# Kernel tuning notes

Measured on AMD Instinct MI355X. Metric: run time of the kernel, lower is better.

## Reference

```python
import jax, jax.numpy as jnp
import numpy as np

N_NODES = 100000
N_EDGES = 1600000
D_IN = 128
D_HID = 128
GARMENT_SIZE = 80000


def setup_inputs() -> dict:
    key = jax.random.key(0)
    k1, k2, k3, k4, k5, k6 = jax.random.split(key, 6)
    notes = jax.random.normal(k1, (N_NODES, D_IN), dtype=jnp.float32)
    w = jax.random.normal(k2, (D_IN, D_HID), dtype=jnp.float32) * 0.05
    b = jax.random.normal(k3, (D_HID,), dtype=jnp.float32) * 0.05
    edge_src = jax.random.randint(k4, (N_EDGES,), 0, N_NODES, dtype=jnp.int32)
    edge_dst = jax.random.randint(k5, (N_EDGES,), 0, N_NODES, dtype=jnp.int32)
    edge_w = jax.random.uniform(k6, (N_EDGES,), dtype=jnp.float32)
    return {
        "notes": notes,
        "w": w,
        "b": b,
        "edge_src": edge_src,
        "edge_dst": edge_dst,
        "edge_w": edge_w,
        "garment_size": GARMENT_SIZE,
    }


def reference(notes, w, b, edge_src, edge_dst, edge_w, garment_size):
    # Dense projection: X0 = notes @ w   -> [N, H]
    X0 = jnp.einsum("nd,dh->nh", notes, w)
    # edge_convolution_template(edge_function=lambda x, y: y, reduction='weighted'):
    # X1[i] = sum over edges (i -> j) of a_ij * X0[j]
    msgs = X0[edge_dst] * edge_w[:, None]                      # [E, H] gather + scale
    X1 = jax.ops.segment_sum(msgs, edge_src, num_segments=notes.shape[0])  # [N, H]
    X = X1 + b
    # concat(act(X), X0[garment_size:]) along node axis -> [2N - garment_size, H]
    return jnp.concatenate([jax.nn.relu(X), X0[garment_size:]], axis=0)
```

## Files before the change

### kernel.cpp

```cpp
#include <hip/hip_runtime.h>

#define H 128
#define NPB 256
#define NB_MAX 1024
#define FILL_CH 4096

static __device__ __forceinline__ unsigned short f2bf(float f) {
  unsigned u = __float_as_uint(f);
  u += 0x7FFFu + ((u >> 16) & 1u);
  return (unsigned short)(u >> 16);
}

__global__ __launch_bounds__(256) void gemm_kernel(
    const float* __restrict__ notes, const float* __restrict__ w,
    const int* __restrict__ g_ptr, unsigned short* __restrict__ x0h,
    float* __restrict__ out, int n_nodes) {
  __shared__ float wtile[32 * H];
  __shared__ float ntile[64 * 32];
  const int tid = threadIdx.x;
  const int tx = tid & 31;
  const int ty = tid >> 5;
  const int rowBlk = blockIdx.x * 64;
  const int g = *g_ptr;

  float acc[8][4];
#pragma unroll
  for (int i = 0; i < 8; ++i)
#pragma unroll
    for (int j = 0; j < 4; ++j) acc[i][j] = 0.f;

  for (int kc = 0; kc < H; kc += 32) {
    __syncthreads();
    {
      const float4* wg = (const float4*)(w + (size_t)kc * H);
      float4* wl = (float4*)wtile;
#pragma unroll
      for (int i = 0; i < 4; ++i) wl[tid + i * 256] = wg[tid + i * 256];
    }
    {
      float4* nl = (float4*)ntile;
#pragma unroll
      for (int i = 0; i < 2; ++i) {
        const int idx = tid + i * 256;
        const int row = idx >> 3;
        const int q = idx & 7;
        const int rr = min(rowBlk + row, n_nodes - 1);
        nl[idx] = *(const float4*)(notes + (size_t)rr * H + kc + q * 4);
      }
    }
    __syncthreads();
#pragma unroll 8
    for (int kk = 0; kk < 32; ++kk) {
      const float4 b4 = *(const float4*)&wtile[kk * H + tx * 4];
      float a[8];
#pragma unroll
      for (int i = 0; i < 8; ++i) a[i] = ntile[(ty * 8 + i) * 32 + kk];
#pragma unroll
      for (int i = 0; i < 8; ++i) {
        acc[i][0] += a[i] * b4.x;
        acc[i][1] += a[i] * b4.y;
        acc[i][2] += a[i] * b4.z;
        acc[i][3] += a[i] * b4.w;
      }
    }
  }

#pragma unroll
  for (int i = 0; i < 8; ++i) {
    const int r = rowBlk + ty * 8 + i;
    if (r < n_nodes) {
      ushort4 h;
      h.x = f2bf(acc[i][0]);
      h.y = f2bf(acc[i][1]);
      h.z = f2bf(acc[i][2]);
      h.w = f2bf(acc[i][3]);
      *(ushort4*)(x0h + (size_t)r * H + tx * 4) = h;
      if (r >= g) {
        float4 v;
        v.x = acc[i][0]; v.y = acc[i][1]; v.z = acc[i][2]; v.w = acc[i][3];
        *(float4*)(out + (size_t)(n_nodes + r - g) * H + tx * 4) = v;
      }
    }
  }
}

__global__ __launch_bounds__(256) void bucket_count_kernel(
    const int* __restrict__ esrc, int* __restrict__ bucketCount, int n_edges,
    int nb) {
  __shared__ int cnt[NB_MAX];
  for (int i = threadIdx.x; i < nb; i += 256) cnt[i] = 0;
  __syncthreads();
  int i = blockIdx.x * 256 + threadIdx.x;
  const int stride = gridDim.x * 256;
  for (; i < n_edges; i += stride) atomicAdd(&cnt[esrc[i] >> 8], 1);
  __syncthreads();
  for (int j = threadIdx.x; j < nb; j += 256) {
    const int c = cnt[j];
    if (c) atomicAdd(&bucketCount[j], c);
  }
}

__global__ __launch_bounds__(256) void bucket_scan_kernel(
    const int* __restrict__ bucketCount, int* __restrict__ bucketBase,
    int* __restrict__ bucketCursor, int* __restrict__ off, int nb,
    int n_nodes, int n_edges) {
  __shared__ int part[256];
  const int t = threadIdx.x;
  const int K = (nb + 255) / 256;
  const int lo = t * K;
  const int hi = min(lo + K, nb);
  int sum = 0;
  for (int i = lo; i < hi; ++i) sum += bucketCount[i];
  part[t] = sum;
  __syncthreads();
  for (int o = 1; o < 256; o <<= 1) {
    const int tv = (t >= o) ? part[t - o] : 0;
    __syncthreads();
    part[t] += tv;
    __syncthreads();
  }
  int run = (t == 0) ? 0 : part[t - 1];
  for (int i = lo; i < hi; ++i) {
    bucketBase[i] = run;
    bucketCursor[i] = run;
    run += bucketCount[i];
  }
  if (t == 255) {
    bucketBase[nb] = part[255];
    off[n_nodes] = n_edges;
  }
}

__global__ __launch_bounds__(256) void bucket_fill_kernel(
    const int* __restrict__ esrc, const int* __restrict__ edst,
    const float* __restrict__ ew, int* __restrict__ bucketCursor,
    int2* __restrict__ sedge, unsigned char* __restrict__ srcloc, int n_edges,
    int nb) {
  __shared__ int2 stage[FILL_CH];
  __shared__ unsigned short bkt16[FILL_CH];
  __shared__ unsigned char loc8[FILL_CH];
  __shared__ int cntA[NB_MAX];
  __shared__ int lbase[NB_MAX];
  __shared__ int cntC[NB_MAX];
  const int t = threadIdx.x;
  const int base = blockIdx.x * FILL_CH;
  const int edgesInBlock = min(FILL_CH, n_edges - base);

  for (int i = t; i < nb; i += 256) {
    cntA[i] = 0;
    cntC[i] = 0;
  }
  __syncthreads();

  for (int k = 0; k < FILL_CH / 256; ++k) {
    const int e = base + k * 256 + t;
    if (e < n_edges) atomicAdd(&cntA[esrc[e] >> 8], 1);
  }
  __syncthreads();

  {
    __shared__ int part[256];
    const int K = (nb + 255) / 256;
    const int lo = t * K;
    const int hi = min(lo + K, nb);
    int sum = 0;
    for (int i = lo; i < hi; ++i) sum += cntA[i];
    part[t] = sum;
    __syncthreads();
    for (int o = 1; o < 256; o <<= 1) {
      const int tv = (t >= o) ? part[t - o] : 0;
      __syncthreads();
      part[t] += tv;
      __syncthreads();
    }
    int run = (t == 0) ? 0 : part[t - 1];
    for (int i = lo; i < hi; ++i) {
      lbase[i] = run;
      run += cntA[i];
    }
  }
  __syncthreads();
  for (int i = t; i < nb; i += 256) {
    const int c = cntA[i];
    cntA[i] = c ? atomicAdd(&bucketCursor[i], c) : 0;
  }
  __syncthreads();

  for (int k = 0; k < FILL_CH / 256; ++k) {
    const int e = base + k * 256 + t;
    if (e < n_edges) {
      const int s = esrc[e];
      const int b = s >> 8;
      const int r = atomicAdd(&cntC[b], 1);
      const int sp = lbase[b] + r;
      int2 pk;
      pk.x = edst[e];
      pk.y = __float_as_int(ew[e]);
      stage[sp] = pk;
      bkt16[sp] = (unsigned short)b;
      loc8[sp] = (unsigned char)(s & 255);
    }
  }
  __syncthreads();

  for (int j = t; j < edgesInBlock; j += 256) {
    const int b = bkt16[j];
    const int pos = cntA[b] + (j - lbase[b]);
    sedge[pos] = stage[j];
    srcloc[pos] = loc8[j];
  }
}

__global__ __launch_bounds__(256) void bucket_sort_kernel(
    const int* __restrict__ bucketBase, const int2* __restrict__ sedge,
    const unsigned char* __restrict__ srcloc, int2* __restrict__ sedge2,
    int* __restrict__ off, int n_nodes) {
  __shared__ int cnt[NPB];
  __shared__ int nodeOff[NPB];
  const int t = threadIdx.x;
  const int beg = bucketBase[blockIdx.x];
  const int end = bucketBase[blockIdx.x + 1];
  const int nodeBase = blockIdx.x * NPB;
  const int nodesInBucket = min(NPB, n_nodes - nodeBase);

  cnt[t] = 0;
  __syncthreads();
  for (int j = beg + t; j < end; j += 256) atomicAdd(&cnt[srcloc[j]], 1);
  __syncthreads();
  {
    const int v = cnt[t];
    int s = v;
    nodeOff[t] = s;
    __syncthreads();
    for (int o = 1; o < 256; o <<= 1) {
      const int tv = (t >= o) ? nodeOff[t - o] : 0;
      __syncthreads();
      nodeOff[t] += tv;
      __syncthreads();
    }
    nodeOff[t] -= v;
  }
  if (t < nodesInBucket) off[nodeBase + t] = beg + nodeOff[t];
  cnt[t] = 0;
  __syncthreads();
  for (int j = beg + t; j < end; j += 256) {
    const int loc = srcloc[j];
    const int r = atomicAdd(&cnt[loc], 1);
    sedge2[beg + nodeOff[loc] + r] = sedge[j];
  }
}

__global__ __launch_bounds__(256) void gather_kernel(
    const int* __restrict__ off, const int2* __restrict__ sedge,
    const unsigned short* __restrict__ x0h, const float* __restrict__ b,
    float* __restrict__ out, int n_nodes) {
  const int wave = blockIdx.x * (blockDim.x >> 6) + (threadIdx.x >> 6);
  const int lane = threadIdx.x & 63;
  if (wave >= n_nodes) return;
  const int beg = off[wave];
  const int end = off[wave + 1];
  const unsigned* __restrict__ x0u = (const unsigned*)x0h;

  float2 a0 = {0.f, 0.f}, a1 = {0.f, 0.f};
  float2 a2 = {0.f, 0.f}, a3 = {0.f, 0.f};
  int e = beg;
  for (; e + 3 < end; e += 4) {
    const int2 e0 = sedge[e];
    const int2 e1 = sedge[e + 1];
    const int2 e2 = sedge[e + 2];
    const int2 e3 = sedge[e + 3];
    const unsigned u0 = x0u[(size_t)e0.x * 64 + lane];
    const unsigned u1 = x0u[(size_t)e1.x * 64 + lane];
    const unsigned u2 = x0u[(size_t)e2.x * 64 + lane];
    const unsigned u3 = x0u[(size_t)e3.x * 64 + lane];
    const float w0 = __int_as_float(e0.y);
    const float w1 = __int_as_float(e1.y);
    const float w2 = __int_as_float(e2.y);
    const float w3 = __int_as_float(e3.y);
    a0.x += __uint_as_float(u0 << 16) * w0;
    a0.y += __uint_as_float(u0 & 0xFFFF0000u) * w0;
    a1.x += __uint_as_float(u1 << 16) * w1;
    a1.y += __uint_as_float(u1 & 0xFFFF0000u) * w1;
    a2.x += __uint_as_float(u2 << 16) * w2;
    a2.y += __uint_as_float(u2 & 0xFFFF0000u) * w2;
    a3.x += __uint_as_float(u3 << 16) * w3;
    a3.y += __uint_as_float(u3 & 0xFFFF0000u) * w3;
  }
  for (; e < end; ++e) {
    const int2 e0 = sedge[e];
    const unsigned u0 = x0u[(size_t)e0.x * 64 + lane];
    const float w0 = __int_as_float(e0.y);
    a0.x += __uint_as_float(u0 << 16) * w0;
    a0.y += __uint_as_float(u0 & 0xFFFF0000u) * w0;
  }
  const float2 bb = ((const float2*)b)[lane];
  float2 r;
  r.x = fmaxf(a0.x + a1.x + a2.x + a3.x + bb.x, 0.f);
  r.y = fmaxf(a0.y + a1.y + a2.y + a3.y + bb.y, 0.f);
  ((float2*)out)[(size_t)wave * 64 + lane] = r;
}

__global__ __launch_bounds__(256) void scatter_kernel(
    const int* __restrict__ esrc, const int* __restrict__ edst,
    const float* __restrict__ ew, const unsigned short* __restrict__ x0h,
    float* __restrict__ acc, int n_edges) {
  const int lane = threadIdx.x & 63;
  const int waveId = blockIdx.x * (blockDim.x >> 6) + (threadIdx.x >> 6);
  const int nWaves = gridDim.x * (blockDim.x >> 6);
  const unsigned* __restrict__ x0u = (const unsigned*)x0h;
  for (int e = waveId; e < n_edges; e += nWaves) {
    const int s = esrc[e];
    const int d = edst[e];
    const float wt = ew[e];
    const unsigned u = x0u[(size_t)d * 64 + lane];
    float* p = acc + (size_t)s * H + lane * 2;
    atomicAdd(p, __uint_as_float(u << 16) * wt);
    atomicAdd(p + 1, __uint_as_float(u & 0xFFFF0000u) * wt);
  }
}

__global__ __launch_bounds__(256) void epilogue_kernel(
    float* __restrict__ out, const float* __restrict__ b, int n4) {
  const int i = blockIdx.x * blockDim.x + threadIdx.x;
  if (i >= n4) return;
  float4* o4 = (float4*)out;
  const float4* b4 = (const float4*)b;
  float4 v = o4[i];
  const float4 bb = b4[i & 31];
  v.x = fmaxf(v.x + bb.x, 0.f);
  v.y = fmaxf(v.y + bb.y, 0.f);
  v.z = fmaxf(v.z + bb.z, 0.f);
  v.w = fmaxf(v.w + bb.w, 0.f);
  o4[i] = v;
}

extern "C" void kernel_launch(void* const* d_in, const int* in_sizes, int n_in,
                              void* d_out, int out_size, void* d_ws, size_t ws_size,
                              hipStream_t stream) {
  const float* notes = (const float*)d_in[0];
  const float* w     = (const float*)d_in[1];
  const float* b     = (const float*)d_in[2];
  const int*   esrc  = (const int*)d_in[3];
  const int*   edst  = (const int*)d_in[4];
  const float* ew    = (const float*)d_in[5];
  const int*   gptr  = (const int*)d_in[6];

  const int n_nodes = in_sizes[0] / H;
  const int n_edges = in_sizes[3];
  float* out = (float*)d_out;

  const int nb = (n_nodes + NPB - 1) / NPB;

  char* ws = (char*)d_ws;
  size_t p = 0;
  auto alloc = [&](size_t bytes) -> char* {
    char* cur = ws + p;
    p = (p + bytes + 255) & ~(size_t)255;
    return cur;
  };
  unsigned short* x0h = (unsigned short*)alloc((size_t)n_nodes * H * 2);
  int*  bucketCount  = (int*)alloc((size_t)nb * sizeof(int));
  int*  bucketBase   = (int*)alloc(((size_t)nb + 1) * sizeof(int));
  int*  bucketCursor = (int*)alloc((size_t)nb * sizeof(int));
  int*  off          = (int*)alloc(((size_t)n_nodes + 1) * sizeof(int));
  int2* sedge        = (int2*)alloc((size_t)n_edges * sizeof(int2));
  int2* sedge2       = (int2*)alloc((size_t)n_edges * sizeof(int2));
  unsigned char* srcloc = (unsigned char*)alloc((size_t)n_edges);
  const bool ok = (p <= ws_size) && (nb <= NB_MAX);

  gemm_kernel<<<(n_nodes + 63) / 64, 256, 0, stream>>>(notes, w, gptr, x0h, out,
                                                       n_nodes);

  if (ok) {
    hipMemsetAsync(bucketCount, 0, (size_t)nb * sizeof(int), stream);
    bucket_count_kernel<<<256, 256, 0, stream>>>(esrc, bucketCount, n_edges,
                                                 nb);
    bucket_scan_kernel<<<1, 256, 0, stream>>>(bucketCount, bucketBase,
                                              bucketCursor, off, nb, n_nodes,
                                              n_edges);
    bucket_fill_kernel<<<(n_edges + FILL_CH - 1) / FILL_CH, 256, 0, stream>>>(
        esrc, edst, ew, bucketCursor, sedge, srcloc, n_edges, nb);
    bucket_sort_kernel<<<nb, 256, 0, stream>>>(bucketBase, sedge, srcloc,
                                               sedge2, off, n_nodes);
    gather_kernel<<<(n_nodes + 3) / 4, 256, 0, stream>>>(off, sedge2, x0h, b,
                                                         out, n_nodes);
  } else {
    hipMemsetAsync(d_out, 0, (size_t)n_nodes * H * sizeof(float), stream);
    scatter_kernel<<<2048, 256, 0, stream>>>(esrc, edst, ew, x0h, out, n_edges);
    const int n4 = n_nodes * H / 4;
    epilogue_kernel<<<(n4 + 255) / 256, 256, 0, stream>>>(out, b, n4);
  }
}
```

Baseline: 308.8 us.

## Build CSR via per-node degree atomics and direct fill; shuffle-batched gather

Replaces the two-pass bucket sort (block-local staging plus per-bucket sort) with a per-node degree histogram using global atomics, a hierarchical scan into per-node offsets, and a direct scatter of each edge into its CSR slot via an atomic cursor. This removes one full pass over an intermediate edge array and the srcloc buffer, at the cost of many global atomics on random addresses and uncoalesced writes. The gather kernel now loads 64 edge records cooperatively per wave and broadcasts them with shuffles, issuing 8 independent row loads per step to raise memory-level parallelism. The order of edges within a node becomes nondeterministic, so float summation order may vary between runs.

```diff
diff --git a/kernel.cpp b/kernel.cpp
--- a/kernel.cpp
+++ b/kernel.cpp
@@ -2,8 +2,6 @@
 
 #define H 128
 #define NPB 256
-#define NB_MAX 1024
-#define FILL_CH 4096
 
 static __device__ __forceinline__ unsigned short f2bf(float f) {
   unsigned u = __float_as_uint(f);
@@ -84,26 +82,30 @@
   }
 }
 
-__global__ __launch_bounds__(256) void bucket_count_kernel(
-    const int* __restrict__ esrc, int* __restrict__ bucketCount, int n_edges,
-    int nb) {
-  __shared__ int cnt[NB_MAX];
-  for (int i = threadIdx.x; i < nb; i += 256) cnt[i] = 0;
+__global__ __launch_bounds__(256) void deg_count_kernel(
+    const int* __restrict__ esrc, int* __restrict__ deg, int n_edges) {
+  const int i = blockIdx.x * 256 + threadIdx.x;
+  if (i >= n_edges) return;
+  atomicAdd(&deg[esrc[i]], 1);
+}
+
+__global__ __launch_bounds__(256) void bucket_sum_kernel(
+    const int* __restrict__ deg, int* __restrict__ bucketCount, int n_nodes) {
+  __shared__ int red[256];
+  const int t = threadIdx.x;
+  const int node = blockIdx.x * 256 + t;
+  red[t] = (node < n_nodes) ? deg[node] : 0;
   __syncthreads();
-  int i = blockIdx.x * 256 + threadIdx.x;
-  const int stride = gridDim.x * 256;
-  for (; i < n_edges; i += stride) atomicAdd(&cnt[esrc[i] >> 8], 1);
-  __syncthreads();
-  for (int j = threadIdx.x; j < nb; j += 256) {
-    const int c = cnt[j];
-    if (c) atomicAdd(&bucketCount[j], c);
-  }
+  for (int o = 128; o > 0; o >>= 1) {
+    if (t < o) red[t] += red[t + o];
+    __syncthreads();
+  }
+  if (t == 0) bucketCount[blockIdx.x] = red[0];
 }
 
 __global__ __launch_bounds__(256) void bucket_scan_kernel(
     const int* __restrict__ bucketCount, int* __restrict__ bucketBase,
-    int* __restrict__ bucketCursor, int* __restrict__ off, int nb,
-    int n_nodes, int n_edges) {
+    int* __restrict__ off, int nb, int n_nodes, int n_edges) {
   __shared__ int part[256];
   const int t = threadIdx.x;
   const int K = (nb + 255) / 256;
@@ -122,7 +124,6 @@
   int run = (t == 0) ? 0 : part[t - 1];
   for (int i = lo; i < hi; ++i) {
     bucketBase[i] = run;
-    bucketCursor[i] = run;
     run += bucketCount[i];
   }
   if (t == 255) {
@@ -131,123 +132,40 @@
   }
 }
 
-__global__ __launch_bounds__(256) void bucket_fill_kernel(
+__global__ __launch_bounds__(256) void node_off_kernel(
+    const int* __restrict__ deg, const int* __restrict__ bucketBase,
+    int* __restrict__ off, int* __restrict__ cursor, int n_nodes) {
+  __shared__ int sc[256];
+  const int t = threadIdx.x;
+  const int node = blockIdx.x * 256 + t;
+  const int v = (node < n_nodes) ? deg[node] : 0;
+  sc[t] = v;
+  __syncthreads();
+  for (int o = 1; o < 256; o <<= 1) {
+    const int tv = (t >= o) ? sc[t - o] : 0;
+    __syncthreads();
+    sc[t] += tv;
+    __syncthreads();
+  }
+  if (node < n_nodes) {
+    const int o0 = bucketBase[blockIdx.x] + sc[t] - v;
+    off[node] = o0;
+    cursor[node] = o0;
+  }
+}
+
+__global__ __launch_bounds__(256) void direct_fill_kernel(
     const int* __restrict__ esrc, const int* __restrict__ edst,
-    const float* __restrict__ ew, int* __restrict__ bucketCursor,
-    int2* __restrict__ sedge, unsigned char* __restrict__ srcloc, int n_edges,
-    int nb) {
-  __shared__ int2 stage[FILL_CH];
-  __shared__ unsigned short bkt16[FILL_CH];
-  __shared__ unsigned char loc8[FILL_CH];
-  __shared__ int cntA[NB_MAX];
-  __shared__ int lbase[NB_MAX];
-  __shared__ int cntC[NB_MAX];
-  const int t = threadIdx.x;
-  const int base = blockIdx.x * FILL_CH;
-  const int edgesInBlock = min(FILL_CH, n_edges - base);
-
-  for (int i = t; i < nb; i += 256) {
-    cntA[i] = 0;
-    cntC[i] = 0;
-  }
-  __syncthreads();
-
-  for (int k = 0; k < FILL_CH / 256; ++k) {
-    const int e = base + k * 256 + t;
-    if (e < n_edges) atomicAdd(&cntA[esrc[e] >> 8], 1);
-  }
-  __syncthreads();
-
-  {
-    __shared__ int part[256];
-    const int K = (nb + 255) / 256;
-    const int lo = t * K;
-    const int hi = min(lo + K, nb);
-    int sum = 0;
-    for (int i = lo; i < hi; ++i) sum += cntA[i];
-    part[t] = sum;
-    __syncthreads();
-    for (int o = 1; o < 256; o <<= 1) {
-      const int tv = (t >= o) ? part[t - o] : 0;
-      __syncthreads();
-      part[t] += tv;
-      __syncthreads();
-    }
-    int run = (t == 0) ? 0 : part[t - 1];
-    for (int i = lo; i < hi; ++i) {
-      lbase[i] = run;
-      run += cntA[i];
-    }
-  }
-  __syncthreads();
-  for (int i = t; i < nb; i += 256) {
-    const int c = cntA[i];
-    cntA[i] = c ? atomicAdd(&bucketCursor[i], c) : 0;
-  }
-  __syncthreads();
-
-  for (int k = 0; k < FILL_CH / 256; ++k) {
-    const int e = base + k * 256 + t;
-    if (e < n_edges) {
-      const int s = esrc[e];
-      const int b = s >> 8;
-      const int r = atomicAdd(&cntC[b], 1);
-      const int sp = lbase[b] + r;
-      int2 pk;
-      pk.x = edst[e];
-      pk.y = __float_as_int(ew[e]);
-      stage[sp] = pk;
-      bkt16[sp] = (unsigned short)b;
-      loc8[sp] = (unsigned char)(s & 255);
-    }
-  }
-  __syncthreads();
-
-  for (int j = t; j < edgesInBlock; j += 256) {
-    const int b = bkt16[j];
-    const int pos = cntA[b] + (j - lbase[b]);
-    sedge[pos] = stage[j];
-    srcloc[pos] = loc8[j];
-  }
-}
-
-__global__ __launch_bounds__(256) void bucket_sort_kernel(
-    const int* __restrict__ bucketBase, const int2* __restrict__ sedge,
-    const unsigned char* __restrict__ srcloc, int2* __restrict__ sedge2,
-    int* __restrict__ off, int n_nodes) {
-  __shared__ int cnt[NPB];
-  __shared__ int nodeOff[NPB];
-  const int t = threadIdx.x;
-  const int beg = bucketBase[blockIdx.x];
-  const int end = bucketBase[blockIdx.x + 1];
-  const int nodeBase = blockIdx.x * NPB;
-  const int nodesInBucket = min(NPB, n_nodes - nodeBase);
-
-  cnt[t] = 0;
-  __syncthreads();
-  for (int j = beg + t; j < end; j += 256) atomicAdd(&cnt[srcloc[j]], 1);
-  __syncthreads();
-  {
-    const int v = cnt[t];
-    int s = v;
-    nodeOff[t] = s;
-    __syncthreads();
-    for (int o = 1; o < 256; o <<= 1) {
-      const int tv = (t >= o) ? nodeOff[t - o] : 0;
-      __syncthreads();
-      nodeOff[t] += tv;
-      __syncthreads();
-    }
-    nodeOff[t] -= v;
-  }
-  if (t < nodesInBucket) off[nodeBase + t] = beg + nodeOff[t];
-  cnt[t] = 0;
-  __syncthreads();
-  for (int j = beg + t; j < end; j += 256) {
-    const int loc = srcloc[j];
-    const int r = atomicAdd(&cnt[loc], 1);
-    sedge2[beg + nodeOff[loc] + r] = sedge[j];
-  }
+    const float* __restrict__ ew, int* __restrict__ cursor,
+    int2* __restrict__ sedge2, int n_edges) {
+  const int i = blockIdx.x * 256 + threadIdx.x;
+  if (i >= n_edges) return;
+  const int s = esrc[i];
+  const int slot = atomicAdd(&cursor[s], 1);
+  int2 pk;
+  pk.x = edst[i];
+  pk.y = __float_as_int(ew[i]);
+  sedge2[slot] = pk;
 }
 
 __global__ __launch_bounds__(256) void gather_kernel(
@@ -259,44 +177,47 @@
   if (wave >= n_nodes) return;
   const int beg = off[wave];
   const int end = off[wave + 1];
+  const int deg = end - beg;
   const unsigned* __restrict__ x0u = (const unsigned*)x0h;
 
-  float2 a0 = {0.f, 0.f}, a1 = {0.f, 0.f};
-  float2 a2 = {0.f, 0.f}, a3 = {0.f, 0.f};
-  int e = beg;
-  for (; e + 3 < end; e += 4) {
-    const int2 e0 = sedge[e];
-    const int2 e1 = sedge[e + 1];
-    const int2 e2 = sedge[e + 2];
-    const int2 e3 = sedge[e + 3];
-    const unsigned u0 = x0u[(size_t)e0.x * 64 + lane];
-    const unsigned u1 = x0u[(size_t)e1.x * 64 + lane];
-    const unsigned u2 = x0u[(size_t)e2.x * 64 + lane];
-    const unsigned u3 = x0u[(size_t)e3.x * 64 + lane];
-    const float w0 = __int_as_float(e0.y);
-    const float w1 = __int_as_float(e1.y);
-    const float w2 = __int_as_float(e2.y);
-    const float w3 = __int_as_float(e3.y);
-    a0.x += __uint_as_float(u0 << 16) * w0;
-    a0.y += __uint_as_float(u0 & 0xFFFF0000u) * w0;
-    a1.x += __uint_as_float(u1 << 16) * w1;
-    a1.y += __uint_as_float(u1 & 0xFFFF0000u) * w1;
-    a2.x += __uint_as_float(u2 << 16) * w2;
-    a2.y += __uint_as_float(u2 & 0xFFFF0000u) * w2;
-    a3.x += __uint_as_float(u3 << 16) * w3;
-    a3.y += __uint_as_float(u3 & 0xFFFF0000u) * w3;
-  }
-  for (; e < end; ++e) {
-    const int2 e0 = sedge[e];
-    const unsigned u0 = x0u[(size_t)e0.x * 64 + lane];
-    const float w0 = __int_as_float(e0.y);
-    a0.x += __uint_as_float(u0 << 16) * w0;
-    a0.y += __uint_as_float(u0 & 0xFFFF0000u) * w0;
-  }
+  float2 acc[8];
+#pragma unroll
+  for (int j = 0; j < 8; ++j) acc[j] = make_float2(0.f, 0.f);
+
+  for (int base = 0; base < deg; base += 64) {
+    const int m = min(64, deg - base);
+    const int2 md = sedge[beg + base + min(lane, m - 1)];
+    const float mw = __int_as_float(md.y);
+    for (int e = 0; e < m; e += 8) {
+      int d[8];
+      float wv[8];
+#pragma unroll
+      for (int j = 0; j < 8; ++j) {
+        const int idx = e + j;
+        const int src = min(idx, m - 1);
+        d[j] = __shfl(md.x, src);
+        const float wj = __shfl(mw, src);
+        wv[j] = (idx < m) ? wj : 0.f;
+      }
+      unsigned u[8];
+#pragma unroll
+      for (int j = 0; j < 8; ++j) u[j] = x0u[(size_t)d[j] * 64 + lane];
+#pragma unroll
+      for (int j = 0; j < 8; ++j) {
+        acc[j].x += __uint_as_float(u[j] << 16) * wv[j];
+        acc[j].y += __uint_as_float(u[j] & 0xFFFF0000u) * wv[j];
+      }
+    }
+  }
+
   const float2 bb = ((const float2*)b)[lane];
   float2 r;
-  r.x = fmaxf(a0.x + a1.x + a2.x + a3.x + bb.x, 0.f);
-  r.y = fmaxf(a0.y + a1.y + a2.y + a3.y + bb.y, 0.f);
+  r.x = fmaxf(acc[0].x + acc[1].x + acc[2].x + acc[3].x + acc[4].x + acc[5].x +
+                  acc[6].x + acc[7].x + bb.x,
+              0.f);
+  r.y = fmaxf(acc[0].y + acc[1].y + acc[2].y + acc[3].y + acc[4].y + acc[5].y +
+                  acc[6].y + acc[7].y + bb.y,
+              0.f);
   ((float2*)out)[(size_t)wave * 64 + lane] = r;
 }
 
@@ -359,29 +280,28 @@
     return cur;
   };
   unsigned short* x0h = (unsigned short*)alloc((size_t)n_nodes * H * 2);
+  int*  deg          = (int*)alloc((size_t)n_nodes * sizeof(int));
+  int*  cursor       = (int*)alloc((size_t)n_nodes * sizeof(int));
+  int*  off          = (int*)alloc(((size_t)n_nodes + 1) * sizeof(int));
   int*  bucketCount  = (int*)alloc((size_t)nb * sizeof(int));
   int*  bucketBase   = (int*)alloc(((size_t)nb + 1) * sizeof(int));
-  int*  bucketCursor = (int*)alloc((size_t)nb * sizeof(int));
-  int*  off          = (int*)alloc(((size_t)n_nodes + 1) * sizeof(int));
-  int2* sedge        = (int2*)alloc((size_t)n_edges * sizeof(int2));
   int2* sedge2       = (int2*)alloc((size_t)n_edges * sizeof(int2));
-  unsigned char* srcloc = (unsigned char*)alloc((size_t)n_edges);
-  const bool ok = (p <= ws_size) && (nb <= NB_MAX);
+  const bool ok = (p <= ws_size);
 
   gemm_kernel<<<(n_nodes + 63) / 64, 256, 0, stream>>>(notes, w, gptr, x0h, out,
                                                        n_nodes);
 
   if (ok) {
-    hipMemsetAsync(bucketCount, 0, (size_t)nb * sizeof(int), stream);
-    bucket_count_kernel<<<256, 256, 0, stream>>>(esrc, bucketCount, n_edges,
-                                                 nb);
-    bucket_scan_kernel<<<1, 256, 0, stream>>>(bucketCount, bucketBase,
-                                              bucketCursor, off, nb, n_nodes,
-                                              n_edges);
-    bucket_fill_kernel<<<(n_edges + FILL_CH - 1) / FILL_CH, 256, 0, stream>>>(
-        esrc, edst, ew, bucketCursor, sedge, srcloc, n_edges, nb);
-    bucket_sort_kernel<<<nb, 256, 0, stream>>>(bucketBase, sedge, srcloc,
-                                               sedge2, off, n_nodes);
+    const int eblocks = (n_edges + 255) / 256;
+    hipMemsetAsync(deg, 0, (size_t)n_nodes * sizeof(int), stream);
+    deg_count_kernel<<<eblocks, 256, 0, stream>>>(esrc, deg, n_edges);
+    bucket_sum_kernel<<<nb, 256, 0, stream>>>(deg, bucketCount, n_nodes);
+    bucket_scan_kernel<<<1, 256, 0, stream>>>(bucketCount, bucketBase, off, nb,
+                                              n_nodes, n_edges);
+    node_off_kernel<<<nb, 256, 0, stream>>>(deg, bucketBase, off, cursor,
+                                            n_nodes);
+    direct_fill_kernel<<<eblocks, 256, 0, stream>>>(esrc, edst, ew, cursor,
+                                                    sedge2, n_edges);
     gather_kernel<<<(n_nodes + 3) / 4, 256, 0, stream>>>(off, sedge2, x0h, b,
                                                          out, n_nodes);
   } else {
```

After: 395.5 us. +28.1%, slower.
